# Performance work log

Measured on AMD Instinct MI355X. Metric: run time of the kernel, lower is better.

The kernel has to match this reference:

```python
import jax, jax.numpy as jnp
import numpy as np

B, N, E, H = 2, 2048, 1024, 16
HD = E // H  # head_dim = 64


def setup_inputs() -> dict:
    key = jax.random.key(0)
    k1, k2, k3, k4, k5 = jax.random.split(key, 5)
    x = jax.random.normal(k1, (B, N, E), dtype=jnp.float32)
    # per-head Linear(E, 3*HD): stacked weights [H, E, 3*HD] and biases [H, 3*HD]
    Wqkv = jax.random.normal(k2, (H, E, 3 * HD), dtype=jnp.float32) * (1.0 / np.sqrt(E))
    bqkv = jax.random.normal(k3, (H, 3 * HD), dtype=jnp.float32) * 0.01
    Wout = jax.random.normal(k4, (E, E), dtype=jnp.float32) * (1.0 / np.sqrt(E))
    bout = jax.random.normal(k5, (E,), dtype=jnp.float32) * 0.01
    return {"x": x, "Wqkv": Wqkv, "bqkv": bqkv, "Wout": Wout, "bout": bout}


def reference(x, Wqkv, bqkv, Wout, bout):
    # per-head QKV projection, vectorized over heads: [B, H, N, 3*HD]
    proj = jnp.einsum('bne,hef->bhnf', x, Wqkv) + bqkv[None, :, None, :]
    k, q, v = jnp.split(proj, 3, axis=-1)  # each [B, H, N, HD]
    # scores = q @ k^T / sqrt(HD): [B, H, N, N]
    scores = jnp.einsum('bhqd,bhkd->bhqk', q, k) / jnp.sqrt(jnp.asarray(HD, dtype=x.dtype))
    # causal mask (tril)
    causal = jnp.tril(jnp.ones((N, N), dtype=bool))
    scores = jnp.where(causal[None, None, :, :], scores, -jnp.inf)
    attn = jax.nn.softmax(scores, axis=-1)
    sa = jnp.einsum('bhqk,bhkd->bhqd', attn, v)  # [B, H, N, HD]
    # concat heads in order -> [B, N, E]
    sa = jnp.transpose(sa, (0, 2, 1, 3)).reshape(B, N, E)
    return sa @ Wout + bout
```

## Files before the change

### kernel.cpp

```cpp
#include <hip/hip_runtime.h>
#include <hip/hip_bf16.h>

#define Bz 2
#define Nn 2048
#define Ee 1024
#define Hh 16
#define HD 64

typedef unsigned short u16;
typedef unsigned int u32;

typedef __bf16 bf16x8 __attribute__((ext_vector_type(8)));
typedef float f32x4 __attribute__((ext_vector_type(4)));

__device__ __forceinline__ float bf2f(u16 u) {
    u32 v = ((u32)u) << 16;
    return __builtin_bit_cast(float, v);
}
__device__ __forceinline__ u16 f2bf(float f) {
    u32 i = __builtin_bit_cast(u32, f);
    u32 r = (i + 0x7FFFu + ((i >> 16) & 1u)) >> 16;
    return (u16)r;
}
__device__ __forceinline__ u32 pack2(float a, float b) {
    return (u32)f2bf(a) | ((u32)f2bf(b) << 16);
}
__device__ __forceinline__ bf16x8 ld_frag(const u16* p) {
    return __builtin_bit_cast(bf16x8, *(const uint4*)p);
}
__device__ __forceinline__ f32x4 zero4() {
    f32x4 z; z[0]=0.f; z[1]=0.f; z[2]=0.f; z[3]=0.f; return z;
}

__device__ __forceinline__ void async_copy16(const u16* g, u16* l) {
    __builtin_amdgcn_global_load_lds(
        (const __attribute__((address_space(1))) u32*)g,
        (__attribute__((address_space(3))) u32*)l, 16, 0, 0);
}

__global__ void ws_diag(float* out, float code) { out[0] = code; }

__global__ __launch_bounds__(256) void convert_x(
    const float* __restrict__ x, u16* __restrict__ xbf)
{
    size_t idx = ((size_t)blockIdx.x * 256 + threadIdx.x) * 8;
    float4 f0 = *(const float4*)(x + idx);
    float4 f1 = *(const float4*)(x + idx + 4);
    uint4 pk;
    pk.x = pack2(f0.x, f0.y); pk.y = pack2(f0.z, f0.w);
    pk.z = pack2(f1.x, f1.y); pk.w = pack2(f1.z, f1.w);
    *(uint4*)(xbf + idx) = pk;
}

__global__ __launch_bounds__(256) void transpose_f32_bf16(
    const float* __restrict__ src, u16* __restrict__ dst, int R, int C)
{
    const int r0 = blockIdx.x * 64, c0 = blockIdx.y * 64;
    const size_t zoff = (size_t)blockIdx.z * R * C;
    src += zoff; dst += zoff;
    const int tid = threadIdx.x;

    __shared__ float T[64][65];
    {
        int tr = tid >> 2, tc = (tid & 3) * 16;
        const float* s = src + (size_t)(r0 + tr) * C + c0 + tc;
#pragma unroll
        for (int j = 0; j < 4; ++j) {
            float4 v = ((const float4*)s)[j];
            T[tr][tc + 4 * j + 0] = v.x; T[tr][tc + 4 * j + 1] = v.y;
            T[tr][tc + 4 * j + 2] = v.z; T[tr][tc + 4 * j + 3] = v.w;
        }
    }
    __syncthreads();
    {
        int cc = tid >> 2, rr = (tid & 3) * 16;
        u16* d = dst + (size_t)(c0 + cc) * R + r0 + rr;
        u32 w[8];
#pragma unroll
        for (int i = 0; i < 8; ++i)
            w[i] = pack2(T[rr + 2 * i][cc], T[rr + 2 * i + 1][cc]);
        *(uint4*)(d)     = make_uint4(w[0], w[1], w[2], w[3]);
        *(uint4*)(d + 8) = make_uint4(w[4], w[5], w[6], w[7]);
    }
}

__global__ __launch_bounds__(256) void transpose_v(
    const u16* __restrict__ src, u16* __restrict__ dst)
{
    const int n0 = blockIdx.x * 64;
    const size_t z = blockIdx.y;
    src += z * (size_t)Nn * HD;
    dst += z * (size_t)HD * Nn;
    const int tid = threadIdx.x;

    __shared__ u16 T[64][66];
    {
        int tr = tid >> 2, tc = (tid & 3) * 16;
        const u16* s = src + (size_t)(n0 + tr) * HD + tc;
        *(uint4*)&T[tr][tc]     = *(const uint4*)(s);
        *(uint4*)&T[tr][tc + 8] = *(const uint4*)(s + 8);
    }
    __syncthreads();
    {
        int cc = tid >> 2, rr = (tid & 3) * 16;
        u32 w[8];
#pragma unroll
        for (int i = 0; i < 8; ++i)
            w[i] = (u32)T[rr + 2 * i][cc] | ((u32)T[rr + 2 * i + 1][cc] << 16);
        u16* d = dst + (size_t)cc * Nn + n0 + rr;
        *(uint4*)(d)     = make_uint4(w[0], w[1], w[2], w[3]);
        *(uint4*)(d + 8) = make_uint4(w[4], w[5], w[6], w[7]);
    }
}

__global__ __launch_bounds__(256) void qkv_mfma(
    const u16* __restrict__ xbf, const u16* __restrict__ Wt,
    const float* __restrict__ bias,
    u16* __restrict__ kbuf, u16* __restrict__ qbuf, u16* __restrict__ vbuf)
{
    const int mt = blockIdx.x;
    const int h  = blockIdx.y;
    const int tid = threadIdx.x;
    const int lane = tid & 63, wid = tid >> 6;
    const int quad = lane >> 4, l15 = lane & 15;

    __shared__ u16 As[64 * 64];
    __shared__ u16 Bs[192 * 64];

    f32x4 acc[4][3];
#pragma unroll
    for (int mi = 0; mi < 4; ++mi)
#pragma unroll
        for (int ni = 0; ni < 3; ++ni) acc[mi][ni] = zero4();

    const u16* xb = xbf + (size_t)mt * 64 * Ee;
    const u16* wtb = Wt + (size_t)h * 192 * 1024;

    const int arowl = lane >> 3;
    const int jj = (lane & 7) ^ arowl;

    for (int kb = 0; kb < 16; ++kb) {
        __syncthreads();
#pragma unroll
        for (int i = 0; i < 2; ++i) {
            int rbase = (wid * 2 + i) * 8;
            const u16* g = xb + (size_t)(rbase + arowl) * Ee + kb * 64 + jj * 8;
            async_copy16(g, &As[(wid * 2 + i) * 512]);
        }
#pragma unroll
        for (int i = 0; i < 6; ++i) {
            int rbase = (wid * 6 + i) * 8;
            const u16* g = wtb + (size_t)(rbase + arowl) * 1024 + kb * 64 + jj * 8;
            async_copy16(g, &Bs[(wid * 6 + i) * 512]);
        }
        __syncthreads();

#pragma unroll
        for (int kk0 = 0; kk0 < 2; ++kk0) {
            const int pos = ((kk0 * 4 + quad) ^ (l15 & 7)) * 8;
            bf16x8 af[4], bf[3];
#pragma unroll
            for (int mi = 0; mi < 4; ++mi)
                af[mi] = ld_frag(&As[(mi * 16 + l15) * 64 + pos]);
#pragma unroll
            for (int ni = 0; ni < 3; ++ni)
                bf[ni] = ld_frag(&Bs[(wid * 48 + ni * 16 + l15) * 64 + pos]);
#pragma unroll
            for (int mi = 0; mi < 4; ++mi)
#pragma unroll
                for (int ni = 0; ni < 3; ++ni)
                    acc[mi][ni] = __builtin_amdgcn_mfma_f32_16x16x32_bf16(
                        af[mi], bf[ni], acc[mi][ni], 0, 0, 0);
        }
    }

#pragma unroll
    for (int ni = 0; ni < 3; ++ni) {
        int col = wid * 48 + ni * 16 + l15;
        int ft = col >> 6, d = col & 63;
        u16* dst = (ft == 0) ? kbuf : (ft == 1) ? qbuf : vbuf;
        float bv = bias[h * 192 + col];
#pragma unroll
        for (int mi = 0; mi < 4; ++mi)
#pragma unroll
            for (int r = 0; r < 4; ++r) {
                int gm = mt * 64 + mi * 16 + quad * 4 + r;
                int bb = gm >> 11, n = gm & (Nn - 1);
                dst[(((size_t)(bb * Hh + h)) * Nn + n) * HD + d] =
                    f2bf(acc[mi][ni][r] + bv);
            }
    }
}

__global__ __launch_bounds__(256) void attn2(
    const u16* __restrict__ qbuf, const u16* __restrict__ kbuf,
    const u16* __restrict__ vtb, u16* __restrict__ sabuf)
{
    const int p  = blockIdx.x;
    const int bh = blockIdx.y;
    const int b = bh >> 4, h = bh & 15;
    const int tid = threadIdx.x;
    const int lane = tid & 63, wid = tid >> 6;
    const int l15 = lane & 15, quad = lane >> 4;

    __shared__ u16 KsL[2][4096];
    __shared__ u16 VtL[2][4096];

    const u16* qb = qbuf + (size_t)bh * Nn * HD;
    const u16* kb = kbuf + (size_t)bh * Nn * HD;
    const u16* vt = vtb + (size_t)bh * HD * Nn;

    const int r_l = lane >> 3;
    const int jj = (lane & 7) ^ r_l;
    const int xsw = l15 & 7;

    const int src0 = l15 + (quad & 1) * 32;
    const bool qhi = quad >= 2;

    const float SC = 0.18033688f;

    for (int hx = 0; hx < 2; ++hx) {
        const int qt = hx ? (31 - p) : p;
        const int nkt = qt + 1;
        const int qrow = qt * 64 + wid * 16 + l15;

        bf16x8 qf[2];
#pragma unroll
        for (int st = 0; st < 2; ++st)
            qf[st] = __builtin_bit_cast(bf16x8,
                *(const uint4*)(qb + (size_t)qrow * HD + st * 32 + quad * 8));

        f32x4 oacc[4];
#pragma unroll
        for (int dt = 0; dt < 4; ++dt) oacc[dt] = zero4();
        float m_i = -3e38f, l_i = 0.f;

        __syncthreads();
#pragma unroll
        for (int i = 0; i < 4; ++i) {
            int idx = wid * 4 + i;
            if (idx < 8) {
                const u16* g = kb + (size_t)(idx * 8 + r_l) * HD + jj * 8;
                async_copy16(g, &KsL[0][idx * 512]);
            } else {
                int ii = idx - 8;
                const u16* g = vt + (size_t)(ii * 8 + r_l) * Nn + jj * 8;
                async_copy16(g, &VtL[0][ii * 512]);
            }
        }

        for (int kt = 0; kt < nkt; ++kt) {
            __syncthreads();
            if (kt + 1 < nkt) {
                const int nb = (kt + 1) & 1;
#pragma unroll
                for (int i = 0; i < 4; ++i) {
                    int idx = wid * 4 + i;
                    if (idx < 8) {
                        const u16* g = kb + (size_t)((kt + 1) * 64 + idx * 8 + r_l) * HD + jj * 8;
                        async_copy16(g, &KsL[nb][idx * 512]);
                    } else {
                        int ii = idx - 8;
                        const u16* g = vt + (size_t)(ii * 8 + r_l) * Nn + (kt + 1) * 64 + jj * 8;
                        async_copy16(g, &VtL[nb][ii * 512]);
                    }
                }
            }
            const u16* K = KsL[kt & 1];
            const u16* V = VtL[kt & 1];

            f32x4 s[4];
#pragma unroll
            for (int t = 0; t < 4; ++t) {
                f32x4 a = zero4();
#pragma unroll
                for (int st = 0; st < 2; ++st) {
                    bf16x8 kf = ld_frag(&K[(t * 16 + l15) * 64 +
                                           ((st * 4 + quad) ^ xsw) * 8]);
                    a = __builtin_amdgcn_mfma_f32_16x16x32_bf16(kf, qf[st], a, 0, 0, 0);
                }
                s[t] = a;
            }

            const bool dn = (kt == qt);
#pragma unroll
            for (int t = 0; t < 4; ++t)
#pragma unroll
                for (int r = 0; r < 4; ++r) {
                    int key = kt * 64 + t * 16 + quad * 4 + r;
                    float v = s[t][r] * SC;
                    if (dn && key > qrow) v = -3e38f;
                    s[t][r] = v;
                }

            float mx = s[0][0];
#pragma unroll
            for (int t = 0; t < 4; ++t)
#pragma unroll
                for (int r = 0; r < 4; ++r) mx = fmaxf(mx, s[t][r]);
            mx = fmaxf(mx, __shfl_xor(mx, 16));
            mx = fmaxf(mx, __shfl_xor(mx, 32));
            float mn = fmaxf(m_i, mx);
            float alpha = exp2f(m_i - mn);
            m_i = mn;
            float rs = 0.f;
#pragma unroll
            for (int t = 0; t < 4; ++t)
#pragma unroll
                for (int r = 0; r < 4; ++r) {
                    float e = exp2f(s[t][r] - mn);
                    s[t][r] = e;
                    rs += e;
                }
            rs += __shfl_xor(rs, 16);
            rs += __shfl_xor(rs, 32);
            l_i = l_i * alpha + rs;
#pragma unroll
            for (int dt = 0; dt < 4; ++dt)
#pragma unroll
                for (int r = 0; r < 4; ++r) oacc[dt][r] *= alpha;

            u32 pk[4][2];
#pragma unroll
            for (int t = 0; t < 4; ++t) {
                pk[t][0] = pack2(s[t][0], s[t][1]);
                pk[t][1] = pack2(s[t][2], s[t][3]);
            }
#pragma unroll
            for (int st = 0; st < 2; ++st) {
                u32 e0 = pk[2 * st][0],     e1 = pk[2 * st][1];
                u32 o0 = pk[2 * st + 1][0], o1 = pk[2 * st + 1][1];
                u32 A0 = __shfl(e0, src0),      B0 = __shfl(o0, src0);
                u32 A1 = __shfl(e1, src0),      B1 = __shfl(o1, src0);
                u32 A2 = __shfl(e0, src0 + 16), B2 = __shfl(o0, src0 + 16);
                u32 A3 = __shfl(e1, src0 + 16), B3 = __shfl(o1, src0 + 16);
                u32 U0 = qhi ? B0 : A0;
                u32 U1 = qhi ? B1 : A1;
                u32 U2 = qhi ? B2 : A2;
                u32 U3 = qhi ? B3 : A3;
                bf16x8 pf = __builtin_bit_cast(bf16x8, make_uint4(U0, U1, U2, U3));
#pragma unroll
                for (int dt = 0; dt < 4; ++dt) {
                    bf16x8 vf = ld_frag(&V[(dt * 16 + l15) * 64 +
                                           ((st * 4 + quad) ^ xsw) * 8]);
                    oacc[dt] = __builtin_amdgcn_mfma_f32_16x16x32_bf16(
                        vf, pf, oacc[dt], 0, 0, 0);
                }
            }
        }

        float inv = 1.f / l_i;
#pragma unroll
        for (int dt = 0; dt < 4; ++dt) {
            ushort4 ov;
            ov.x = f2bf(oacc[dt][0] * inv);
            ov.y = f2bf(oacc[dt][1] * inv);
            ov.z = f2bf(oacc[dt][2] * inv);
            ov.w = f2bf(oacc[dt][3] * inv);
            *(ushort4*)&sabuf[((size_t)(b * Nn + qrow)) * Ee + h * 64 +
                              dt * 16 + quad * 4] = ov;
        }
    }
}

typedef float f32x16 __attribute__((ext_vector_type(16)));
__device__ __forceinline__ f32x16 zero16() {
    f32x16 z;
#pragma unroll
    for (int i = 0; i < 16; ++i) z[i] = 0.f;
    return z;
}

__global__ __launch_bounds__(256) void out_mfma(
    const u16* __restrict__ A, const u16* __restrict__ Wt,
    const float* __restrict__ bias, float* __restrict__ out)
{
    const int mt = blockIdx.x;
    const int nt = blockIdx.y;
    const int tid = threadIdx.x;
    const int lane = tid & 63, wid = tid >> 6;
    const int l31 = lane & 31, khalf = (lane >> 5) * 8;

    __shared__ u16 As[128][72];
    __shared__ u16 Bs[64][72];

    f32x16 acc[2];
    acc[0] = zero16(); acc[1] = zero16();

    const u16* ab = A + (size_t)mt * 128 * Ee;
    const int arow = tid >> 1, akh = (tid & 1) * 32;
    const int brow = tid >> 2, bc = (tid & 3) * 16;

    for (int k0 = 0; k0 < Ee; k0 += 64) {
        __syncthreads();
        {
            const u16* asrc = ab + (size_t)arow * Ee + k0 + akh;
#pragma unroll
            for (int j = 0; j < 4; ++j)
                *(uint4*)&As[arow][akh + 8 * j] = *(const uint4*)(asrc + 8 * j);
            const u16* bsrc = Wt + (size_t)(nt * 64 + brow) * 1024 + k0 + bc;
            *(uint4*)&Bs[brow][bc]     = *(const uint4*)(bsrc);
            *(uint4*)&Bs[brow][bc + 8] = *(const uint4*)(bsrc + 8);
        }
        __syncthreads();
#pragma unroll
        for (int kc = 0; kc < 4; ++kc) {
            bf16x8 af = ld_frag(&As[wid * 32 + l31][kc * 16 + khalf]);
#pragma unroll
            for (int ct = 0; ct < 2; ++ct) {
                bf16x8 bf = ld_frag(&Bs[ct * 32 + l31][kc * 16 + khalf]);
                acc[ct] = __builtin_amdgcn_mfma_f32_32x32x16_bf16(af, bf, acc[ct], 0, 0, 0);
            }
        }
    }

#pragma unroll
    for (int ct = 0; ct < 2; ++ct) {
        int col = nt * 64 + ct * 32 + l31;
        float bv = bias[col];
#pragma unroll
        for (int r = 0; r < 16; ++r) {
            int row_l = (r & 3) + 8 * (r >> 2) + 4 * (lane >> 5);
            int gm = mt * 128 + wid * 32 + row_l;
            out[(size_t)gm * Ee + col] = acc[ct][r] + bv;
        }
    }
}

extern "C" void kernel_launch(void* const* d_in, const int* in_sizes, int n_in,
                              void* d_out, int out_size, void* d_ws, size_t ws_size,
                              hipStream_t stream) {
    const float* x    = (const float*)d_in[0];
    const float* Wqkv = (const float*)d_in[1];
    const float* bqkv = (const float*)d_in[2];
    const float* Wout = (const float*)d_in[3];
    const float* bout = (const float*)d_in[4];
    float* out = (float*)d_out;

    const size_t SZ = (size_t)Bz * Hh * Nn * HD;
    const size_t NSA = (size_t)Bz * Nn * Ee;
    const size_t NEED = (3 * SZ + NSA) * sizeof(u16);

    if (ws_size < NEED) {
        ws_diag<<<1, 1, 0, stream>>>(out, 20000.0f + (float)(ws_size >> 20));
        return;
    }

    u16* ws = (u16*)d_ws;
    u16* kbuf  = ws;
    u16* qbuf  = ws + SZ;
    u16* vbuf  = ws + 2 * SZ;
    u16* sabuf = ws + 3 * SZ;
    u16* wqkv_t = sabuf;
    u16* wout_t = kbuf;
    u16* xbf    = (u16*)d_out;
    u16* vtb    = (u16*)d_out + SZ;

    convert_x<<<2048, 256, 0, stream>>>(x, xbf);
    transpose_f32_bf16<<<dim3(16, 3, 16), 256, 0, stream>>>(Wqkv, wqkv_t, 1024, 192);
    qkv_mfma<<<dim3(64, 16), 256, 0, stream>>>(xbf, wqkv_t, bqkv, kbuf, qbuf, vbuf);
    transpose_v<<<dim3(32, 32), 256, 0, stream>>>(vbuf, vtb);
    attn2<<<dim3(16, 32), 256, 0, stream>>>(qbuf, kbuf, vtb, sabuf);
    transpose_f32_bf16<<<dim3(16, 16, 1), 256, 0, stream>>>(Wout, wout_t, 1024, 1024);
    out_mfma<<<dim3(32, 16), 256, 0, stream>>>(sabuf, wout_t, bout, out);
}
```

Measured before the change: 210.5 us.

## Shrink attention query tiles to 32 rows with 2-wave blocks and swizzled grid

The attention kernel now uses 128-thread blocks, each handling a 32-row query tile instead of 64. The launch doubles to 1024 blocks, with a 1-D grid remapped so neighbouring blocks work on different batch-heads. Causal masking runs only on the last key tile, and the other tiles just apply the scale. The aim is more blocks for better CU occupancy and load balance. The cost is that K/V tiles are loaded by half as many waves and reused across fewer query rows, which roughly doubles K/V traffic per query.

Result: no change. 212.1 us (+0.8%).

```diff
diff --git a/kernel.cpp b/kernel.cpp
--- a/kernel.cpp
+++ b/kernel.cpp
@@ -192,12 +192,13 @@
     }
 }
 
-__global__ __launch_bounds__(256) void attn2(
+__global__ __launch_bounds__(128) void attn2(
     const u16* __restrict__ qbuf, const u16* __restrict__ kbuf,
     const u16* __restrict__ vtb, u16* __restrict__ sabuf)
 {
-    const int p  = blockIdx.x;
-    const int bh = blockIdx.y;
+    const int id = blockIdx.x;
+    const int bh = (id & 7) * 4 + ((id >> 3) & 3);
+    const int p  = id >> 5;
     const int b = bh >> 4, h = bh & 15;
     const int tid = threadIdx.x;
     const int lane = tid & 63, wid = tid >> 6;
@@ -220,9 +221,9 @@
     const float SC = 0.18033688f;
 
     for (int hx = 0; hx < 2; ++hx) {
-        const int qt = hx ? (31 - p) : p;
-        const int nkt = qt + 1;
-        const int qrow = qt * 64 + wid * 16 + l15;
+        const int qt = hx ? (63 - p) : p;
+        const int nkt = (qt + 2) >> 1;
+        const int qrow = qt * 32 + wid * 16 + l15;
 
         bf16x8 qf[2];
 #pragma unroll
@@ -237,15 +238,13 @@
 
         __syncthreads();
 #pragma unroll
-        for (int i = 0; i < 4; ++i) {
-            int idx = wid * 4 + i;
-            if (idx < 8) {
-                const u16* g = kb + (size_t)(idx * 8 + r_l) * HD + jj * 8;
-                async_copy16(g, &KsL[0][idx * 512]);
+        for (int i = 0; i < 8; ++i) {
+            if (wid == 0) {
+                const u16* g = kb + (size_t)(i * 8 + r_l) * HD + jj * 8;
+                async_copy16(g, &KsL[0][i * 512]);
             } else {
-                int ii = idx - 8;
-                const u16* g = vt + (size_t)(ii * 8 + r_l) * Nn + jj * 8;
-                async_copy16(g, &VtL[0][ii * 512]);
+                const u16* g = vt + (size_t)(i * 8 + r_l) * Nn + jj * 8;
+                async_copy16(g, &VtL[0][i * 512]);
             }
         }
 
@@ -254,15 +253,13 @@
             if (kt + 1 < nkt) {
                 const int nb = (kt + 1) & 1;
 #pragma unroll
-                for (int i = 0; i < 4; ++i) {
-                    int idx = wid * 4 + i;
-                    if (idx < 8) {
-                        const u16* g = kb + (size_t)((kt + 1) * 64 + idx * 8 + r_l) * HD + jj * 8;
-                        async_copy16(g, &KsL[nb][idx * 512]);
+                for (int i = 0; i < 8; ++i) {
+                    if (wid == 0) {
+                        const u16* g = kb + (size_t)((kt + 1) * 64 + i * 8 + r_l) * HD + jj * 8;
+                        async_copy16(g, &KsL[nb][i * 512]);
                     } else {
-                        int ii = idx - 8;
-                        const u16* g = vt + (size_t)(ii * 8 + r_l) * Nn + (kt + 1) * 64 + jj * 8;
-                        async_copy16(g, &VtL[nb][ii * 512]);
+                        const u16* g = vt + (size_t)(i * 8 + r_l) * Nn + (kt + 1) * 64 + jj * 8;
+                        async_copy16(g, &VtL[nb][i * 512]);
                     }
                 }
             }
@@ -282,16 +279,22 @@
                 s[t] = a;
             }
 
-            const bool dn = (kt == qt);
-#pragma unroll
-            for (int t = 0; t < 4; ++t)
-#pragma unroll
-                for (int r = 0; r < 4; ++r) {
-                    int key = kt * 64 + t * 16 + quad * 4 + r;
-                    float v = s[t][r] * SC;
-                    if (dn && key > qrow) v = -3e38f;
-                    s[t][r] = v;
-                }
+            if (kt == nkt - 1) {
+#pragma unroll
+                for (int t = 0; t < 4; ++t)
+#pragma unroll
+                    for (int r = 0; r < 4; ++r) {
+                        int key = kt * 64 + t * 16 + quad * 4 + r;
+                        float v = s[t][r] * SC;
+                        if (key > qrow) v = -3e38f;
+                        s[t][r] = v;
+                    }
+            } else {
+#pragma unroll
+                for (int t = 0; t < 4; ++t)
+#pragma unroll
+                    for (int r = 0; r < 4; ++r) s[t][r] *= SC;
+            }
 
             float mx = s[0][0];
 #pragma unroll
@@ -460,7 +463,7 @@
     transpose_f32_bf16<<<dim3(16, 3, 16), 256, 0, stream>>>(Wqkv, wqkv_t, 1024, 192);
     qkv_mfma<<<dim3(64, 16), 256, 0, stream>>>(xbf, wqkv_t, bqkv, kbuf, qbuf, vbuf);
     transpose_v<<<dim3(32, 32), 256, 0, stream>>>(vbuf, vtb);
-    attn2<<<dim3(16, 32), 256, 0, stream>>>(qbuf, kbuf, vtb, sabuf);
+    attn2<<<dim3(1024), 128, 0, stream>>>(qbuf, kbuf, vtb, sabuf);
     transpose_f32_bf16<<<dim3(16, 16, 1), 256, 0, stream>>>(Wout, wout_t, 1024, 1024);
     out_mfma<<<dim3(32, 16), 256, 0, stream>>>(sabuf, wout_t, bout, out);
 }
```

## Split causal attention KV range across two blocks and merge partials

Applied to the files above, without the earlier changes.

Each query tile's key range is split into two halves handled by separate blocks (1024 blocks instead of 512), each writing unnormalized bf16 partial outputs plus running max and sum. A new merge kernel combines the two partials with log-sum-exp rescaling, and the output GEMM now reads the head-major layout directly. The block index is also remapped to interleave heads. This aims to raise occupancy and balance load on the many-CU GPU, at the cost of an extra kernel launch, extra partial-buffer traffic, and bf16 rounding of unnormalized partials.

Result: faster. 205.4 us (-2.4%).

```diff
diff --git a/kernel.cpp b/kernel.cpp
--- a/kernel.cpp
+++ b/kernel.cpp
@@ -194,11 +194,12 @@
 
 __global__ __launch_bounds__(256) void attn2(
     const u16* __restrict__ qbuf, const u16* __restrict__ kbuf,
-    const u16* __restrict__ vtb, u16* __restrict__ sabuf)
-{
-    const int p  = blockIdx.x;
-    const int bh = blockIdx.y;
-    const int b = bh >> 4, h = bh & 15;
+    const u16* __restrict__ vtb, u16* __restrict__ p0buf,
+    u16* __restrict__ p1buf, float* __restrict__ ml)
+{
+    const int id = blockIdx.x;
+    const int bh = (id & 7) * 4 + ((id >> 3) & 3);
+    const int p  = id >> 5;
     const int tid = threadIdx.x;
     const int lane = tid & 63, wid = tid >> 6;
     const int l15 = lane & 15, quad = lane >> 4;
@@ -213,154 +214,200 @@
     const int r_l = lane >> 3;
     const int jj = (lane & 7) ^ r_l;
     const int xsw = l15 & 7;
-
     const int src0 = l15 + (quad & 1) * 32;
     const bool qhi = quad >= 2;
-
     const float SC = 0.18033688f;
 
-    for (int hx = 0; hx < 2; ++hx) {
-        const int qt = hx ? (31 - p) : p;
-        const int nkt = qt + 1;
+    for (int sg = 0; sg < 2; ++sg) {
+        const int qt = sg ? (31 - p) : p;
+        const int T  = qt + 1;
+        const int t0 = sg ? ((T + 1) >> 1) : 0;
+        const int t1 = sg ? T : ((p + 2) >> 1);
+        u16*   pb = sg ? p1buf : p0buf;
+        float* mb = ml + (sg ? 131072 : 0);
+        float* lb = ml + (sg ? 196608 : 65536);
+
         const int qrow = qt * 64 + wid * 16 + l15;
-
-        bf16x8 qf[2];
-#pragma unroll
-        for (int st = 0; st < 2; ++st)
-            qf[st] = __builtin_bit_cast(bf16x8,
-                *(const uint4*)(qb + (size_t)qrow * HD + st * 32 + quad * 8));
 
         f32x4 oacc[4];
 #pragma unroll
         for (int dt = 0; dt < 4; ++dt) oacc[dt] = zero4();
         float m_i = -3e38f, l_i = 0.f;
 
-        __syncthreads();
-#pragma unroll
-        for (int i = 0; i < 4; ++i) {
-            int idx = wid * 4 + i;
-            if (idx < 8) {
-                const u16* g = kb + (size_t)(idx * 8 + r_l) * HD + jj * 8;
-                async_copy16(g, &KsL[0][idx * 512]);
-            } else {
-                int ii = idx - 8;
-                const u16* g = vt + (size_t)(ii * 8 + r_l) * Nn + jj * 8;
-                async_copy16(g, &VtL[0][ii * 512]);
+        if (t0 < t1) {
+            bf16x8 qf[2];
+#pragma unroll
+            for (int st = 0; st < 2; ++st)
+                qf[st] = __builtin_bit_cast(bf16x8,
+                    *(const uint4*)(qb + (size_t)qrow * HD + st * 32 + quad * 8));
+
+            __syncthreads();
+#pragma unroll
+            for (int i2 = 0; i2 < 4; ++i2) {
+                int idx = wid * 4 + i2;
+                if (idx < 8) {
+                    const u16* g = kb + (size_t)(t0 * 64 + idx * 8 + r_l) * HD + jj * 8;
+                    async_copy16(g, &KsL[0][idx * 512]);
+                } else {
+                    int ii = idx - 8;
+                    const u16* g = vt + (size_t)(ii * 8 + r_l) * Nn + t0 * 64 + jj * 8;
+                    async_copy16(g, &VtL[0][ii * 512]);
+                }
             }
-        }
-
-        for (int kt = 0; kt < nkt; ++kt) {
-            __syncthreads();
-            if (kt + 1 < nkt) {
-                const int nb = (kt + 1) & 1;
-#pragma unroll
-                for (int i = 0; i < 4; ++i) {
-                    int idx = wid * 4 + i;
-                    if (idx < 8) {
-                        const u16* g = kb + (size_t)((kt + 1) * 64 + idx * 8 + r_l) * HD + jj * 8;
-                        async_copy16(g, &KsL[nb][idx * 512]);
-                    } else {
-                        int ii = idx - 8;
-                        const u16* g = vt + (size_t)(ii * 8 + r_l) * Nn + (kt + 1) * 64 + jj * 8;
-                        async_copy16(g, &VtL[nb][ii * 512]);
+
+            const int nit = t1 - t0;
+            for (int i = 0; i < nit; ++i) {
+                const int tk = t0 + i;
+                __syncthreads();
+                if (i + 1 < nit) {
+                    const int nb = (i + 1) & 1;
+#pragma unroll
+                    for (int i2 = 0; i2 < 4; ++i2) {
+                        int idx = wid * 4 + i2;
+                        if (idx < 8) {
+                            const u16* g = kb + (size_t)((tk + 1) * 64 + idx * 8 + r_l) * HD + jj * 8;
+                            async_copy16(g, &KsL[nb][idx * 512]);
+                        } else {
+                            int ii = idx - 8;
+                            const u16* g = vt + (size_t)(ii * 8 + r_l) * Nn + (tk + 1) * 64 + jj * 8;
+                            async_copy16(g, &VtL[nb][ii * 512]);
+                        }
+                    }
+                }
+                const u16* K = KsL[i & 1];
+                const u16* V = VtL[i & 1];
+
+                f32x4 s[4];
+#pragma unroll
+                for (int t = 0; t < 4; ++t) {
+                    f32x4 a = zero4();
+#pragma unroll
+                    for (int st = 0; st < 2; ++st) {
+                        bf16x8 kf = ld_frag(&K[(t * 16 + l15) * 64 +
+                                               ((st * 4 + quad) ^ xsw) * 8]);
+                        a = __builtin_amdgcn_mfma_f32_16x16x32_bf16(kf, qf[st], a, 0, 0, 0);
+                    }
+                    s[t] = a;
+                }
+
+                if (tk == qt) {
+#pragma unroll
+                    for (int t = 0; t < 4; ++t)
+#pragma unroll
+                        for (int r = 0; r < 4; ++r) {
+                            int key = tk * 64 + t * 16 + quad * 4 + r;
+                            float v = s[t][r] * SC;
+                            if (key > qrow) v = -3e38f;
+                            s[t][r] = v;
+                        }
+                } else {
+#pragma unroll
+                    for (int t = 0; t < 4; ++t)
+#pragma unroll
+                        for (int r = 0; r < 4; ++r) s[t][r] *= SC;
+                }
+
+                float mx = s[0][0];
+#pragma unroll
+                for (int t = 0; t < 4; ++t)
+#pragma unroll
+                    for (int r = 0; r < 4; ++r) mx = fmaxf(mx, s[t][r]);
+                mx = fmaxf(mx, __shfl_xor(mx, 16));
+                mx = fmaxf(mx, __shfl_xor(mx, 32));
+                float mn = fmaxf(m_i, mx);
+                float alpha = exp2f(m_i - mn);
+                m_i = mn;
+                float rs = 0.f;
+#pragma unroll
+                for (int t = 0; t < 4; ++t)
+#pragma unroll
+                    for (int r = 0; r < 4; ++r) {
+                        float e = exp2f(s[t][r] - mn);
+                        s[t][r] = e;
+                        rs += e;
+                    }
+                rs += __shfl_xor(rs, 16);
+                rs += __shfl_xor(rs, 32);
+                l_i = l_i * alpha + rs;
+#pragma unroll
+                for (int dt = 0; dt < 4; ++dt)
+#pragma unroll
+                    for (int r = 0; r < 4; ++r) oacc[dt][r] *= alpha;
+
+                u32 pk[4][2];
+#pragma unroll
+                for (int t = 0; t < 4; ++t) {
+                    pk[t][0] = pack2(s[t][0], s[t][1]);
+                    pk[t][1] = pack2(s[t][2], s[t][3]);
+                }
+#pragma unroll
+                for (int st = 0; st < 2; ++st) {
+                    u32 e0 = pk[2 * st][0],     e1 = pk[2 * st][1];
+                    u32 o0 = pk[2 * st + 1][0], o1 = pk[2 * st + 1][1];
+                    u32 A0 = __shfl(e0, src0),      B0 = __shfl(o0, src0);
+                    u32 A1 = __shfl(e1, src0),      B1 = __shfl(o1, src0);
+                    u32 A2 = __shfl(e0, src0 + 16), B2 = __shfl(o0, src0 + 16);
+                    u32 A3 = __shfl(e1, src0 + 16), B3 = __shfl(o1, src0 + 16);
+                    u32 U0 = qhi ? B0 : A0;
+                    u32 U1 = qhi ? B1 : A1;
+                    u32 U2 = qhi ? B2 : A2;
+                    u32 U3 = qhi ? B3 : A3;
+                    bf16x8 pf = __builtin_bit_cast(bf16x8, make_uint4(U0, U1, U2, U3));
+#pragma unroll
+                    for (int dt = 0; dt < 4; ++dt) {
+                        bf16x8 vf = ld_frag(&V[(dt * 16 + l15) * 64 +
+                                               ((st * 4 + quad) ^ xsw) * 8]);
+                        oacc[dt] = __builtin_amdgcn_mfma_f32_16x16x32_bf16(
+                            vf, pf, oacc[dt], 0, 0, 0);
                     }
                 }
             }
-            const u16* K = KsL[kt & 1];
-            const u16* V = VtL[kt & 1];
-
-            f32x4 s[4];
-#pragma unroll
-            for (int t = 0; t < 4; ++t) {
-                f32x4 a = zero4();
-#pragma unroll
-                for (int st = 0; st < 2; ++st) {
-                    bf16x8 kf = ld_frag(&K[(t * 16 + l15) * 64 +
-                                           ((st * 4 + quad) ^ xsw) * 8]);
-                    a = __builtin_amdgcn_mfma_f32_16x16x32_bf16(kf, qf[st], a, 0, 0, 0);
-                }
-                s[t] = a;
-            }
-
-            const bool dn = (kt == qt);
-#pragma unroll
-            for (int t = 0; t < 4; ++t)
-#pragma unroll
-                for (int r = 0; r < 4; ++r) {
-                    int key = kt * 64 + t * 16 + quad * 4 + r;
-                    float v = s[t][r] * SC;
-                    if (dn && key > qrow) v = -3e38f;
-                    s[t][r] = v;
-                }
-
-            float mx = s[0][0];
-#pragma unroll
-            for (int t = 0; t < 4; ++t)
-#pragma unroll
-                for (int r = 0; r < 4; ++r) mx = fmaxf(mx, s[t][r]);
-            mx = fmaxf(mx, __shfl_xor(mx, 16));
-            mx = fmaxf(mx, __shfl_xor(mx, 32));
-            float mn = fmaxf(m_i, mx);
-            float alpha = exp2f(m_i - mn);
-            m_i = mn;
-            float rs = 0.f;
-#pragma unroll
-            for (int t = 0; t < 4; ++t)
-#pragma unroll
-                for (int r = 0; r < 4; ++r) {
-                    float e = exp2f(s[t][r] - mn);
-                    s[t][r] = e;
-                    rs += e;
-                }
-            rs += __shfl_xor(rs, 16);
-            rs += __shfl_xor(rs, 32);
-            l_i = l_i * alpha + rs;
-#pragma unroll
-            for (int dt = 0; dt < 4; ++dt)
-#pragma unroll
-                for (int r = 0; r < 4; ++r) oacc[dt][r] *= alpha;
-
-            u32 pk[4][2];
-#pragma unroll
-            for (int t = 0; t < 4; ++t) {
-                pk[t][0] = pack2(s[t][0], s[t][1]);
-                pk[t][1] = pack2(s[t][2], s[t][3]);
-            }
-#pragma unroll
-            for (int st = 0; st < 2; ++st) {
-                u32 e0 = pk[2 * st][0],     e1 = pk[2 * st][1];
-                u32 o0 = pk[2 * st + 1][0], o1 = pk[2 * st + 1][1];
-                u32 A0 = __shfl(e0, src0),      B0 = __shfl(o0, src0);
-                u32 A1 = __shfl(e1, src0),      B1 = __shfl(o1, src0);
-                u32 A2 = __shfl(e0, src0 + 16), B2 = __shfl(o0, src0 + 16);
-                u32 A3 = __shfl(e1, src0 + 16), B3 = __shfl(o1, src0 + 16);
-                u32 U0 = qhi ? B0 : A0;
-                u32 U1 = qhi ? B1 : A1;
-                u32 U2 = qhi ? B2 : A2;
-                u32 U3 = qhi ? B3 : A3;
-                bf16x8 pf = __builtin_bit_cast(bf16x8, make_uint4(U0, U1, U2, U3));
-#pragma unroll
-                for (int dt = 0; dt < 4; ++dt) {
-                    bf16x8 vf = ld_frag(&V[(dt * 16 + l15) * 64 +
-                                           ((st * 4 + quad) ^ xsw) * 8]);
-                    oacc[dt] = __builtin_amdgcn_mfma_f32_16x16x32_bf16(
-                        vf, pf, oacc[dt], 0, 0, 0);
-                }
-            }
-        }
-
-        float inv = 1.f / l_i;
+        }
+
 #pragma unroll
         for (int dt = 0; dt < 4; ++dt) {
             ushort4 ov;
-            ov.x = f2bf(oacc[dt][0] * inv);
-            ov.y = f2bf(oacc[dt][1] * inv);
-            ov.z = f2bf(oacc[dt][2] * inv);
-            ov.w = f2bf(oacc[dt][3] * inv);
-            *(ushort4*)&sabuf[((size_t)(b * Nn + qrow)) * Ee + h * 64 +
-                              dt * 16 + quad * 4] = ov;
-        }
-    }
+            ov.x = f2bf(oacc[dt][0]);
+            ov.y = f2bf(oacc[dt][1]);
+            ov.z = f2bf(oacc[dt][2]);
+            ov.w = f2bf(oacc[dt][3]);
+            *(ushort4*)&pb[((size_t)bh * Nn + qrow) * HD + dt * 16 + quad * 4] = ov;
+        }
+        if (quad == 0) {
+            mb[bh * Nn + qrow] = m_i;
+            lb[bh * Nn + qrow] = l_i;
+        }
+    }
+}
+
+__global__ __launch_bounds__(256) void attn_merge(
+    const u16* __restrict__ p0, u16* __restrict__ p1,
+    const float* __restrict__ ml)
+{
+    const int idx = blockIdx.x * 256 + threadIdx.x;
+    const int row = idx >> 3;
+    const int dc = (idx & 7) * 8;
+
+    const float m1 = ml[row],          l1 = ml[65536 + row];
+    const float m2 = ml[131072 + row], l2 = ml[196608 + row];
+    const float m = fmaxf(m1, m2);
+    const float a1 = exp2f(m1 - m), a2 = exp2f(m2 - m);
+    const float inv = 1.f / (a1 * l1 + a2 * l2);
+    const float s1 = a1 * inv, s2 = a2 * inv;
+
+    const size_t off = (size_t)row * HD + dc;
+    uint4 v0 = *(const uint4*)&p0[off];
+    uint4 v1 = *(const uint4*)&p1[off];
+    u32 a[4] = {v0.x, v0.y, v0.z, v0.w};
+    u32 b[4] = {v1.x, v1.y, v1.z, v1.w};
+    u32 w[4];
+#pragma unroll
+    for (int j = 0; j < 4; ++j) {
+        float x0 = bf2f((u16)a[j]) * s1 + bf2f((u16)b[j]) * s2;
+        float x1 = bf2f((u16)(a[j] >> 16)) * s1 + bf2f((u16)(b[j] >> 16)) * s2;
+        w[j] = pack2(x0, x1);
+    }
+    *(uint4*)&p1[off] = make_uint4(w[0], w[1], w[2], w[3]);
 }
 
 typedef float f32x16 __attribute__((ext_vector_type(16)));
@@ -387,14 +434,17 @@
     f32x16 acc[2];
     acc[0] = zero16(); acc[1] = zero16();
 
-    const u16* ab = A + (size_t)mt * 128 * Ee;
     const int arow = tid >> 1, akh = (tid & 1) * 32;
+    const int gm = mt * 128 + arow;
+    const int bb = gm >> 11, n = gm & (Nn - 1);
     const int brow = tid >> 2, bc = (tid & 3) * 16;
 
     for (int k0 = 0; k0 < Ee; k0 += 64) {
         __syncthreads();
         {
-            const u16* asrc = ab + (size_t)arow * Ee + k0 + akh;
+            const int c = k0 + akh;
+            const int h = c >> 6, d0 = c & 63;
+            const u16* asrc = A + (((size_t)(bb * Hh + h) * Nn + n) * HD + d0);
 #pragma unroll
             for (int j = 0; j < 4; ++j)
                 *(uint4*)&As[arow][akh + 8 * j] = *(const uint4*)(asrc + 8 * j);
@@ -421,8 +471,8 @@
 #pragma unroll
         for (int r = 0; r < 16; ++r) {
             int row_l = (r & 3) + 8 * (r >> 2) + 4 * (lane >> 5);
-            int gm = mt * 128 + wid * 32 + row_l;
-            out[(size_t)gm * Ee + col] = acc[ct][r] + bv;
+            int gm2 = mt * 128 + wid * 32 + row_l;
+            out[(size_t)gm2 * Ee + col] = acc[ct][r] + bv;
         }
     }
 }
@@ -455,12 +505,16 @@
     u16* wout_t = kbuf;
     u16* xbf    = (u16*)d_out;
     u16* vtb    = (u16*)d_out + SZ;
+    u16* p0     = (u16*)d_out;
+    u16* p1     = vbuf;
+    float* ml   = (float*)sabuf;
 
     convert_x<<<2048, 256, 0, stream>>>(x, xbf);
     transpose_f32_bf16<<<dim3(16, 3, 16), 256, 0, stream>>>(Wqkv, wqkv_t, 1024, 192);
     qkv_mfma<<<dim3(64, 16), 256, 0, stream>>>(xbf, wqkv_t, bqkv, kbuf, qbuf, vbuf);
     transpose_v<<<dim3(32, 32), 256, 0, stream>>>(vbuf, vtb);
-    attn2<<<dim3(16, 32), 256, 0, stream>>>(qbuf, kbuf, vtb, sabuf);
+    attn2<<<dim3(1024), 256, 0, stream>>>(qbuf, kbuf, vtb, p0, p1, ml);
+    attn_merge<<<dim3(2048), 256, 0, stream>>>(p0, p1, ml);
     transpose_f32_bf16<<<dim3(16, 16, 1), 256, 0, stream>>>(Wout, wout_t, 1024, 1024);
-    out_mfma<<<dim3(32, 16), 256, 0, stream>>>(sabuf, wout_t, bout, out);
-}
+    out_mfma<<<dim3(32, 16), 256, 0, stream>>>(p1, wout_t, bout, out);
+}
```
